# Kernel optimization log

Hardware: AMD Instinct MI355X
Metric: run time of the kernel (lower is better)

Reference implementation:

```python
import jax, jax.numpy as jnp
import numpy as np

# TT config (matches init_kwargs)
NUM_TABLES = 4
P = (100, 100, 100)          # tt_p_shapes, prod = num_embeddings = 1e6
Q = (4, 4, 4)                # tt_q_shapes, prod = embedding_dim = 64
R = (1, 32, 32, 1)           # tt_ranks with boundary ranks
BAGS_PER_TABLE = 8192
POOL = 16                    # indices per bag


def setup_inputs() -> dict:
    key = jax.random.key(0)
    k1, k2, k3, k4 = jax.random.split(key, 4)
    nnz = NUM_TABLES * BAGS_PER_TABLE * POOL      # 524288
    B = NUM_TABLES * BAGS_PER_TABLE               # 32768 bags total
    indices = jax.random.randint(k1, (nnz,), 0, P[0] * P[1] * P[2], dtype=jnp.int64)
    offsets = (jnp.arange(B + 1, dtype=jnp.int64) * POOL)
    scale = 0.05  # small init, akin to approx-normal weight_dist
    tt_core_0 = jax.random.normal(k2, (NUM_TABLES, P[0], R[0] * Q[0] * R[1]), dtype=jnp.float32) * scale
    tt_core_1 = jax.random.normal(k3, (NUM_TABLES, P[1], R[1] * Q[1] * R[2]), dtype=jnp.float32) * scale
    tt_core_2 = jax.random.normal(k4, (NUM_TABLES, P[2], R[2] * Q[2] * R[3]), dtype=jnp.float32) * scale
    return {"indices": indices, "offsets": offsets,
            "tt_core_0": tt_core_0, "tt_core_1": tt_core_1, "tt_core_2": tt_core_2}


def reference(indices, offsets, tt_core_0, tt_core_1, tt_core_2):
    nnz = indices.shape[0]
    B = offsets.shape[0] - 1
    bags_per_table = B // NUM_TABLES

    # bag id for each nonzero (embedding-bag semantics), then table id per nonzero
    rowidx = jnp.searchsorted(offsets, jnp.arange(nnz, dtype=offsets.dtype), side='right') - 1
    tableidx = rowidx // bags_per_table

    # decompose flat row index into TT indices (C-order over p-shapes,
    # matching tt_matrix_to_full row layout)
    i0 = indices // (P[1] * P[2])
    i1 = (indices // P[2]) % P[1]
    i2 = indices % P[2]

    # gather per-lookup core slices
    c0 = tt_core_0[tableidx, i0].reshape(nnz, Q[0], R[1])          # r0 == 1
    c1 = tt_core_1[tableidx, i1].reshape(nnz, R[1], Q[1], R[2])
    c2 = tt_core_2[tableidx, i2].reshape(nnz, R[2], Q[2])          # r3 == 1

    # on-the-fly TT contraction to reconstruct embedding rows [nnz, D]
    t = jnp.einsum('nar,nrbs->nabs', c0, c1)                       # [nnz, q0, q1, r2]
    rows = jnp.einsum('nabs,nsc->nabc', t, c2).reshape(nnz, Q[0] * Q[1] * Q[2])

    # sum-pool per bag
    out = jax.ops.segment_sum(rows, rowidx, num_segments=B)        # [B, D]
    return out
```

## Files before the change

### kernel.cpp

```cpp
#include <hip/hip_runtime.h>
#include <stdint.h>

#define NT 4
#define PP 100
#define TT_BYTES (4ull * 100 * 100 * 1024)


__device__ __forceinline__ uint32_t f2bf(float f) {
    union { float f; uint32_t u; } v; v.f = f;
    uint32_t u = v.u;
    return (u + 0x7fffu + ((u >> 16) & 1u)) >> 16;
}

__device__ __forceinline__ float dot2bf(uint32_t a, uint32_t b, float c) {
    float d;
    asm("v_dot2_f32_bf16 %0, %1, %2, %3" : "=v"(d) : "v"(a), "v"(b), "v"(c));
    return d;
}

__global__ __launch_bounds__(256)
void c2pack_kernel(const float* __restrict__ c2g, uint32_t* __restrict__ c2p) {
    int t = blockIdx.x * 256 + threadIdx.x;
    if (t >= NT * PP * 64) return;
    int c = t & 3, sg = (t >> 2) & 15, rest = t >> 6;
    int i2 = rest % PP, tab = rest / PP;
    const float* src = c2g + (size_t)(tab * PP + i2) * 128;
    float e = src[(2 * sg) * 4 + c];
    float o = src[(2 * sg + 1) * 4 + c];
    c2p[t] = f2bf(e) | (f2bf(o) << 16);
}

__global__ __launch_bounds__(128, 3)
void tt_phase1(const float* __restrict__ c0g, const float* __restrict__ c1g,
               unsigned short* __restrict__ tT) {
    __shared__ float c1s[32 * 128];
    __shared__ float c0t[16 * 132];

    int blk = blockIdx.x;
    int tab   = blk / 700;
    int rem   = blk % 700;
    int i1    = rem / 7;
    int chunk = rem % 7;
    int i0_base = chunk * 16;
    int tid = threadIdx.x;

    const float4* c1p = (const float4*)(c1g + (size_t)(tab * PP + i1) * 4096);
    float4* c1v = (float4*)c1s;
    #pragma unroll
    for (int it = 0; it < 8; ++it) c1v[tid + 128 * it] = c1p[tid + 128 * it];

    #pragma unroll
    for (int it = 0; it < 16; ++it) {
        int f = tid + 128 * it;
        int i0l = f >> 7;
        int x   = f & 127;
        int a = x >> 5, r = x & 31;
        int i0 = i0_base + i0l; if (i0 > PP - 1) i0 = PP - 1;
        c0t[i0l * 132 + r * 4 + a] = c0g[(size_t)(tab * PP + i0) * 128 + x];
    }
    __syncthreads();

    int u  = tid >> 4;
    int sg = tid & 15;

    float acc[2][2][16];
    #pragma unroll
    for (int ii = 0; ii < 2; ++ii)
        #pragma unroll
        for (int e = 0; e < 2; ++e)
            #pragma unroll
            for (int q = 0; q < 16; ++q) acc[ii][e][q] = 0.f;

    #pragma unroll 4
    for (int r = 0; r < 32; ++r) {
        float4 av0 = *(const float4*)&c0t[(2 * u) * 132 + r * 4];
        float4 av1 = *(const float4*)&c0t[(2 * u + 1) * 132 + r * 4];
        const float* a0 = (const float*)&av0;
        const float* a1 = (const float*)&av1;
        #pragma unroll
        for (int b = 0; b < 4; ++b) {
            float2 bv = *(const float2*)&c1s[r * 128 + b * 32 + 2 * sg];
            #pragma unroll
            for (int a = 0; a < 4; ++a) {
                acc[0][0][a * 4 + b] += a0[a] * bv.x;
                acc[0][1][a * 4 + b] += a0[a] * bv.y;
                acc[1][0][a * 4 + b] += a1[a] * bv.x;
                acc[1][1][a * 4 + b] += a1[a] * bv.y;
            }
        }
    }

    #pragma unroll
    for (int ii = 0; ii < 2; ++ii) {
        int i0 = i0_base + 2 * u + ii;
        if (i0 >= PP) continue;
        size_t combo = (size_t)tab * 10000 + (size_t)i0 * 100 + (size_t)i1;
        char* base = (char*)tT + combo * 1024 + (size_t)sg * 64;
        #pragma unroll
        for (int k = 0; k < 4; ++k) {
            uint4 w;
            w.x = f2bf(acc[ii][0][4*k+0]) | (f2bf(acc[ii][1][4*k+0]) << 16);
            w.y = f2bf(acc[ii][0][4*k+1]) | (f2bf(acc[ii][1][4*k+1]) << 16);
            w.z = f2bf(acc[ii][0][4*k+2]) | (f2bf(acc[ii][1][4*k+2]) << 16);
            w.w = f2bf(acc[ii][0][4*k+3]) | (f2bf(acc[ii][1][4*k+3]) << 16);
            *(uint4*)(base + k * 16) = w;
        }
    }
}

__global__ __launch_bounds__(256, 3)
void tt_phase2(const int* __restrict__ indices, const int* __restrict__ offsets,
               const unsigned short* __restrict__ tT, const uint32_t* __restrict__ c2p,
               float* __restrict__ out, int bags_per_table, int B) {
    int lane = threadIdx.x & 63;
    int wv   = threadIdx.x >> 6;
    int bag  = blockIdx.x * 4 + wv;
    if (bag >= B) return;
    int sub = lane >> 4;
    int sg  = lane & 15;
    int tab = bag / bags_per_table;
    int start = offsets[bag];

    const uint4* c2q = (const uint4*)c2p;

    const uint4* tp[4];
    int ci[4];
    #pragma unroll
    for (int j = 0; j < 4; ++j) {
        uint32_t idx = (uint32_t)indices[start + j * 4 + sub];
        uint32_t i0 = idx / 10000u;
        uint32_t r1 = idx - i0 * 10000u;
        uint32_t i1 = r1 / 100u;
        uint32_t i2 = r1 - i1 * 100u;
        tp[j] = (const uint4*)((const char*)tT +
                 ((size_t)tab * 10000u + i0 * 100u + i1) * 1024 + (size_t)sg * 64);
        ci[j] = (tab * PP + (int)i2) * 16 + sg;
    }

    uint4 T[4][4];
    uint4 C[4];
    #pragma unroll
    for (int j = 0; j < 4; ++j) {
        T[j][0] = tp[j][0]; T[j][1] = tp[j][1];
        T[j][2] = tp[j][2]; T[j][3] = tp[j][3];
        C[j] = c2q[ci[j]];
    }

    float acc[64];
    #pragma unroll
    for (int d = 0; d < 64; ++d) acc[d] = 0.f;

    #pragma unroll
    for (int j = 0; j < 4; ++j) {
        uint32_t cd[4] = { C[j].x, C[j].y, C[j].z, C[j].w };
        #pragma unroll
        for (int k = 0; k < 4; ++k) {
            uint32_t td[4] = { T[j][k].x, T[j][k].y, T[j][k].z, T[j][k].w };
            #pragma unroll
            for (int m = 0; m < 4; ++m) {
                int d0 = (4 * k + m) * 4;
                acc[d0 + 0] = dot2bf(td[m], cd[0], acc[d0 + 0]);
                acc[d0 + 1] = dot2bf(td[m], cd[1], acc[d0 + 1]);
                acc[d0 + 2] = dot2bf(td[m], cd[2], acc[d0 + 2]);
                acc[d0 + 3] = dot2bf(td[m], cd[3], acc[d0 + 3]);
            }
        }
    }

    #pragma unroll
    for (int m = 32; m >= 1; m >>= 1) {
        bool up = (lane & m) != 0;
        #pragma unroll
        for (int j = 0; j < m; ++j) {
            float lo = acc[j], hi = acc[j + m];
            float send = up ? lo : hi;
            float recv = __shfl_xor(send, m, 64);
            acc[j] = (up ? hi : lo) + recv;
        }
    }
    out[(size_t)bag * 64 + lane] = acc[0];
}

extern "C" void kernel_launch(void* const* d_in, const int* in_sizes, int n_in,
                              void* d_out, int out_size, void* d_ws, size_t ws_size,
                              hipStream_t stream) {
    const int*   indices = (const int*)d_in[0];
    const int*   offsets = (const int*)d_in[1];
    const float* c0      = (const float*)d_in[2];
    const float* c1      = (const float*)d_in[3];
    const float* c2      = (const float*)d_in[4];
    float* out = (float*)d_out;

    int B = in_sizes[1] - 1;
    int bags_per_table = B / NT;

    unsigned short* tT  = (unsigned short*)d_ws;
    uint32_t*       c2p = (uint32_t*)((char*)d_ws + TT_BYTES);

    c2pack_kernel<<<dim3((NT * PP * 64 + 255) / 256), dim3(256), 0, stream>>>(c2, c2p);
    tt_phase1<<<dim3(NT * PP * 7), dim3(128), 0, stream>>>(c0, c1, tT);
    tt_phase2<<<dim3((B + 3) / 4), dim3(256), 0, stream>>>(indices, offsets, tT, c2p, out,
                                                           bags_per_table, B);
}
```

Measured before the change: 155.9 us.

## Use MFMA bf16 matrix ops for per-bag TT contraction with relaid intermediates

Phase 2 replaces the per-lane v_dot2 accumulation and 64-register shuffle reduction with a 16x16x32 bf16 MFMA per lookup. Each lookup's precomputed core0*core1 slab becomes the A operand, and the matching core2 slice becomes the B operand. The phase-1 output layout and the core2 packing are reordered so each lane loads contiguous 16-byte operand fragments, and the bag sum happens inside the MFMA accumulator. This removes the heavy shuffle reduction and cuts register pressure, so occupancy can rise to 4 blocks per unit. In exchange, phase 1 now issues scattered 4-byte stores instead of 16-byte ones.

```diff
diff --git a/kernel.cpp b/kernel.cpp
--- a/kernel.cpp
+++ b/kernel.cpp
@@ -4,7 +4,11 @@
 #define NT 4
 #define PP 100
 #define TT_BYTES (4ull * 100 * 100 * 1024)
+#define C2B_DWORDS (NT * PP * 64)
 
+
+typedef short bf16x8 __attribute__((ext_vector_type(8)));
+typedef float f32x4  __attribute__((ext_vector_type(4)));
 
 __device__ __forceinline__ uint32_t f2bf(float f) {
     union { float f; uint32_t u; } v; v.f = f;
@@ -12,22 +16,13 @@
     return (u + 0x7fffu + ((u >> 16) & 1u)) >> 16;
 }
 
-__device__ __forceinline__ float dot2bf(uint32_t a, uint32_t b, float c) {
-    float d;
-    asm("v_dot2_f32_bf16 %0, %1, %2, %3" : "=v"(d) : "v"(a), "v"(b), "v"(c));
-    return d;
-}
-
 __global__ __launch_bounds__(256)
 void c2pack_kernel(const float* __restrict__ c2g, uint32_t* __restrict__ c2p) {
     int t = blockIdx.x * 256 + threadIdx.x;
-    if (t >= NT * PP * 64) return;
-    int c = t & 3, sg = (t >> 2) & 15, rest = t >> 6;
-    int i2 = rest % PP, tab = rest / PP;
-    const float* src = c2g + (size_t)(tab * PP + i2) * 128;
-    float e = src[(2 * sg) * 4 + c];
-    float o = src[(2 * sg + 1) * 4 + c];
-    c2p[t] = f2bf(e) | (f2bf(o) << 16);
+    if (t >= C2B_DWORDS) return;
+    int sg = t & 15, c = (t >> 4) & 3, combo = t >> 6;
+    const float* src = c2g + (size_t)combo * 128;
+    c2p[t] = f2bf(src[(2 * sg) * 4 + c]) | (f2bf(src[(2 * sg + 1) * 4 + c]) << 16);
 }
 
 __global__ __launch_bounds__(128, 3)
@@ -95,90 +90,61 @@
         int i0 = i0_base + 2 * u + ii;
         if (i0 >= PP) continue;
         size_t combo = (size_t)tab * 10000 + (size_t)i0 * 100 + (size_t)i1;
-        char* base = (char*)tT + combo * 1024 + (size_t)sg * 64;
+        char* base = (char*)tT + combo * 1024 + (size_t)sg * 4;
         #pragma unroll
-        for (int k = 0; k < 4; ++k) {
-            uint4 w;
-            w.x = f2bf(acc[ii][0][4*k+0]) | (f2bf(acc[ii][1][4*k+0]) << 16);
-            w.y = f2bf(acc[ii][0][4*k+1]) | (f2bf(acc[ii][1][4*k+1]) << 16);
-            w.z = f2bf(acc[ii][0][4*k+2]) | (f2bf(acc[ii][1][4*k+2]) << 16);
-            w.w = f2bf(acc[ii][0][4*k+3]) | (f2bf(acc[ii][1][4*k+3]) << 16);
-            *(uint4*)(base + k * 16) = w;
+        for (int ab = 0; ab < 16; ++ab) {
+            uint32_t w = f2bf(acc[ii][0][ab]) | (f2bf(acc[ii][1][ab]) << 16);
+            *(uint32_t*)(base + ab * 64) = w;
         }
     }
 }
 
-__global__ __launch_bounds__(256, 3)
+__global__ __launch_bounds__(256, 4)
 void tt_phase2(const int* __restrict__ indices, const int* __restrict__ offsets,
-               const unsigned short* __restrict__ tT, const uint32_t* __restrict__ c2p,
+               const char* __restrict__ tT, const char* __restrict__ c2b,
                float* __restrict__ out, int bags_per_table, int B) {
     int lane = threadIdx.x & 63;
     int wv   = threadIdx.x >> 6;
     int bag  = blockIdx.x * 4 + wv;
     if (bag >= B) return;
-    int sub = lane >> 4;
-    int sg  = lane & 15;
+    int col = lane & 15;
+    int kq  = lane >> 4;
     int tab = bag / bags_per_table;
     int start = offsets[bag];
 
-    const uint4* c2q = (const uint4*)c2p;
+    uint32_t idx = (uint32_t)indices[start + col];
+    uint32_t i0 = idx / 10000u;
+    uint32_t r1 = idx - i0 * 10000u;
+    uint32_t i1 = r1 / 100u;
+    uint32_t i2 = r1 - i1 * 100u;
+    uint32_t tby = (((uint32_t)tab * 10000u + i0 * 100u + i1) << 10);
+    uint32_t cby = (((uint32_t)tab * 100u + i2) << 8);
 
-    const uint4* tp[4];
-    int ci[4];
+    int aoff = col * 64 + kq * 16;
+    int boff = (col & 3) * 64 + kq * 16;
+
+    bf16x8 A[16];
     #pragma unroll
-    for (int j = 0; j < 4; ++j) {
-        uint32_t idx = (uint32_t)indices[start + j * 4 + sub];
-        uint32_t i0 = idx / 10000u;
-        uint32_t r1 = idx - i0 * 10000u;
-        uint32_t i1 = r1 / 100u;
-        uint32_t i2 = r1 - i1 * 100u;
-        tp[j] = (const uint4*)((const char*)tT +
-                 ((size_t)tab * 10000u + i0 * 100u + i1) * 1024 + (size_t)sg * 64);
-        ci[j] = (tab * PP + (int)i2) * 16 + sg;
+    for (int j = 0; j < 16; ++j) {
+        uint32_t tb = (uint32_t)__builtin_amdgcn_readlane((int)tby, j);
+        A[j] = *(const bf16x8*)(tT + tb + aoff);
     }
 
-    uint4 T[4][4];
-    uint4 C[4];
+    f32x4 acc = {0.f, 0.f, 0.f, 0.f};
     #pragma unroll
-    for (int j = 0; j < 4; ++j) {
-        T[j][0] = tp[j][0]; T[j][1] = tp[j][1];
-        T[j][2] = tp[j][2]; T[j][3] = tp[j][3];
-        C[j] = c2q[ci[j]];
+    for (int j = 0; j < 16; ++j) {
+        uint32_t cb = (uint32_t)__builtin_amdgcn_readlane((int)cby, j);
+        const bf16x8 Bv = *(const bf16x8*)(c2b + cb + boff);
+        acc = __builtin_amdgcn_mfma_f32_16x16x32_bf16(A[j], Bv, acc, 0, 0, 0);
     }
 
-    float acc[64];
-    #pragma unroll
-    for (int d = 0; d < 64; ++d) acc[d] = 0.f;
-
-    #pragma unroll
-    for (int j = 0; j < 4; ++j) {
-        uint32_t cd[4] = { C[j].x, C[j].y, C[j].z, C[j].w };
-        #pragma unroll
-        for (int k = 0; k < 4; ++k) {
-            uint32_t td[4] = { T[j][k].x, T[j][k].y, T[j][k].z, T[j][k].w };
-            #pragma unroll
-            for (int m = 0; m < 4; ++m) {
-                int d0 = (4 * k + m) * 4;
-                acc[d0 + 0] = dot2bf(td[m], cd[0], acc[d0 + 0]);
-                acc[d0 + 1] = dot2bf(td[m], cd[1], acc[d0 + 1]);
-                acc[d0 + 2] = dot2bf(td[m], cd[2], acc[d0 + 2]);
-                acc[d0 + 3] = dot2bf(td[m], cd[3], acc[d0 + 3]);
-            }
-        }
+    if (col < 4) {
+        float* o = out + (size_t)bag * 64 + kq * 16 + col;
+        o[0]  = acc[0];
+        o[4]  = acc[1];
+        o[8]  = acc[2];
+        o[12] = acc[3];
     }
-
-    #pragma unroll
-    for (int m = 32; m >= 1; m >>= 1) {
-        bool up = (lane & m) != 0;
-        #pragma unroll
-        for (int j = 0; j < m; ++j) {
-            float lo = acc[j], hi = acc[j + m];
-            float send = up ? lo : hi;
-            float recv = __shfl_xor(send, m, 64);
-            acc[j] = (up ? hi : lo) + recv;
-        }
-    }
-    out[(size_t)bag * 64 + lane] = acc[0];
 }
 
 extern "C" void kernel_launch(void* const* d_in, const int* in_sizes, int n_in,
@@ -197,8 +163,10 @@
     unsigned short* tT  = (unsigned short*)d_ws;
     uint32_t*       c2p = (uint32_t*)((char*)d_ws + TT_BYTES);
 
-    c2pack_kernel<<<dim3((NT * PP * 64 + 255) / 256), dim3(256), 0, stream>>>(c2, c2p);
+    c2pack_kernel<<<dim3((C2B_DWORDS + 255) / 256), dim3(256), 0, stream>>>(c2, c2p);
     tt_phase1<<<dim3(NT * PP * 7), dim3(128), 0, stream>>>(c0, c1, tT);
-    tt_phase2<<<dim3((B + 3) / 4), dim3(256), 0, stream>>>(indices, offsets, tT, c2p, out,
+    tt_phase2<<<dim3((B + 3) / 4), dim3(256), 0, stream>>>(indices, offsets,
+                                                           (const char*)tT,
+                                                           (const char*)c2p, out,
                                                            bags_per_table, B);
 }
```

Result: no change. 158.0 us (+1.4%).
